# Kernel optimization log

Hardware: AMD Instinct MI355X
Metric: run time of the kernel (lower is better)

Reference implementation:

```python
import jax, jax.numpy as jnp
import numpy as np

N_NODES = 50000
N_EDGES = 1600000
LORA_R = 8


def gcn_conv(h, W, b, src, dst, n):
    # PyG GCNConv: linear transform, add self-loops, symmetric normalization,
    # scatter-add aggregation at target nodes, then bias.
    h = h @ W  # [N, out]
    ones = jnp.ones(src.shape[0], dtype=h.dtype)
    deg = jax.ops.segment_sum(ones, dst, num_segments=n) + 1.0  # +1 for self-loop
    dis = jax.lax.rsqrt(deg)  # deg >= 1 always
    norm = dis[src] * dis[dst]  # [E]
    agg = jax.ops.segment_sum(norm[:, None] * h[src], dst, num_segments=n)
    agg = agg + (dis * dis)[:, None] * h  # self-loop contribution
    return agg + b


def lora(h, A, B):
    # LoRALinear: b(a(x)) * (1/r); replaces input (not additive)
    return (h @ A) @ B * (1.0 / LORA_R)


def setup_inputs() -> dict:
    key = jax.random.key(0)
    ks = jax.random.split(key, 12)
    inp = {}
    inp['x'] = jax.random.normal(ks[0], (N_NODES, 128), dtype=jnp.float32)
    inp['edge_index'] = jax.random.randint(ks[1], (2, N_EDGES), 0, N_NODES, dtype=jnp.int64 if jax.config.jax_enable_x64 else jnp.int32)
    inp['domain_idx'] = jax.random.randint(ks[2], (N_NODES,), 0, 3, dtype=jnp.int32)
    inp['emb_table'] = jax.random.normal(ks[3], (3, 4096), dtype=jnp.float32)
    s1 = 1.0 / np.sqrt(4224.0)
    inp['W1'] = jax.random.normal(ks[4], (4224, 32), dtype=jnp.float32) * s1
    inp['b1'] = jnp.zeros((32,), dtype=jnp.float32)
    inp['A1'] = jax.random.normal(ks[5], (32, LORA_R), dtype=jnp.float32) * (1.0 / np.sqrt(32.0))
    inp['B1'] = jax.random.normal(ks[6], (LORA_R, 32), dtype=jnp.float32) * (1.0 / np.sqrt(LORA_R))
    inp['W2'] = jax.random.normal(ks[7], (32, 5), dtype=jnp.float32) * (1.0 / np.sqrt(32.0))
    inp['b2'] = jnp.zeros((5,), dtype=jnp.float32)
    inp['A2'] = jax.random.normal(ks[8], (5, LORA_R), dtype=jnp.float32) * (1.0 / np.sqrt(5.0))
    inp['B2'] = jax.random.normal(ks[9], (LORA_R, 5), dtype=jnp.float32) * (1.0 / np.sqrt(LORA_R))
    return inp


def reference(x, edge_index, domain_idx, emb_table, W1, b1, A1, B1, W2, b2, A2, B2):
    n = x.shape[0]
    src, dst = edge_index[0], edge_index[1]
    embedded = emb_table[domain_idx]  # [N, 4096]
    h = jnp.concatenate([embedded, x], axis=1)  # [N, 4224]
    h = gcn_conv(h, W1, b1, src, dst, n)
    h = lora(h, A1, B1)
    h = jax.nn.relu(h)
    h = gcn_conv(h, W2, b2, src, dst, n)
    h = lora(h, A2, B2)
    return jax.nn.log_softmax(h, axis=1)
```

## Files before the change

kernel.cpp:

```cpp
#include <hip/hip_runtime.h>
#include <hip/hip_bf16.h>
#include <hip/hip_fp16.h>


#define XDIM 128
#define ODIM 5
#define EMBDIM 4096
#define TB 8192
#define BSH 6
#define BN 64
#define ECAP2 2560

__global__ void __launch_bounds__(256) k_bin(
    const int* __restrict__ src, const int* __restrict__ dst,
    unsigned int* __restrict__ sorted, int* __restrict__ bcur, int e, int ntiles,
    const float* __restrict__ emb, const float* __restrict__ W1,
    float* __restrict__ emb_part) {
    __shared__ unsigned int staged[TB];
    __shared__ int loff[1024], rctr[1024], sbase[1024];
    int t = threadIdx.x;
    if (blockIdx.x >= ntiles) {
        int bx2 = blockIdx.x - ntiles;
        int dm = bx2 >> 5, seg = bx2 & 31;
        const float* er = emb + dm * EMBDIM + seg * 128;
        const float* wr = W1 + (size_t)seg * 128 * 32;
        int j = t & 31, kk = t >> 5;
        float acc = 0.f;
        for (int k2 = kk; k2 < 128; k2 += 8) acc += er[k2] * wr[k2 * 32 + j];
        float* p = (float*)staged;
        p[kk * 32 + j] = acc;
        __syncthreads();
        if (t < 32) {
            float s = 0.f;
            #pragma unroll
            for (int r = 0; r < 8; ++r) s += p[r * 32 + t];
            emb_part[bx2 * 32 + t] = s;
        }
        return;
    }
    int base = blockIdx.x * TB;
    int len = min(TB, e - base);
    for (int i = t; i < 1024; i += 256) { loff[i] = 0; rctr[i] = 0; }
    __syncthreads();
    for (int i = t; i < len; i += 256) atomicAdd(&loff[dst[base + i] >> BSH], 1);
    __syncthreads();
    if (t < 64) {
        int ch = t * 16;
        int v[16]; int s0 = 0;
        #pragma unroll
        for (int k = 0; k < 16; ++k) { v[k] = loff[ch + k]; s0 += v[k]; }
        int pre = s0;
        #pragma unroll
        for (int d2 = 1; d2 < 64; d2 <<= 1) {
            int up = __shfl_up(pre, d2);
            if (t >= d2) pre += up;
        }
        int excl = pre - s0;
        #pragma unroll
        for (int k = 0; k < 16; ++k) { loff[ch + k] = excl; excl += v[k]; }
    }
    __syncthreads();
    for (int i = t; i < len; i += 256) {
        int s = src[base + i], d = dst[base + i];
        int b = d >> BSH;
        int r = atomicAdd(&rctr[b], 1);
        staged[loff[b] + r] = ((unsigned int)d << 16) | (unsigned int)s;
    }
    __syncthreads();
    for (int b = t; b < 1024; b += 256) {
        int l = ((b < 1023) ? loff[b + 1] : len) - loff[b];
        if (l > 0) sbase[b] = atomicAdd(&bcur[b], l);
    }
    __syncthreads();
    for (int i = t; i < len; i += 256) {
        unsigned int u = staged[i];
        int b = (int)(u >> 22);
        int pos = sbase[b] + (i - loff[b]);
        if (pos < ECAP2) sorted[(size_t)b * ECAP2 + pos] = u;
    }
}

__global__ void __launch_bounds__(256) k_disS(
    const unsigned int* __restrict__ sorted, const int* __restrict__ bcur,
    float* __restrict__ dis, int* __restrict__ deg, int n,
    const float* __restrict__ A1, const float* __restrict__ A2,
    const float* __restrict__ B2, const float* __restrict__ b1,
    const float* __restrict__ emb_part, float* __restrict__ M2,
    float* __restrict__ b1A1, float* __restrict__ emb_proj) {
    __shared__ int h[BN];
    int t = threadIdx.x, b = blockIdx.x;
    if (t < BN) h[t] = 0;
    __syncthreads();
    int m = min(bcur[b], ECAP2);
    const unsigned int* sp = sorted + (size_t)b * ECAP2;
    for (int i = t; i < m; i += 256) {
        int d = (int)(sp[i] >> 16);
        atomicAdd(&h[d & (BN - 1)], 1);
    }
    __syncthreads();
    if (t < BN) {
        int node = (b << BSH) + t;
        if (node < n) {
            deg[node] = h[t];
            dis[node] = rsqrtf((float)(h[t] + 1));
        }
    }
    if (b == 0) {
        if (t < 25) {
            int c = t / 5, cp = t % 5;
            float s = 0.f;
            #pragma unroll
            for (int r = 0; r < 8; ++r) s += A2[c * 8 + r] * B2[r * 5 + cp];
            M2[c * 5 + cp] = s * 0.125f;
        }
        if (t >= 32 && t < 40) {
            int j = t - 32;
            float s = 0.f;
            #pragma unroll
            for (int k = 0; k < 32; ++k) s += b1[k] * A1[k * 8 + j];
            b1A1[j] = s;
        }
        if (t >= 64 && t < 160) {
            int d = (t - 64) >> 5, j = (t - 64) & 31;
            float s = 0.f;
            #pragma unroll
            for (int seg = 0; seg < 32; ++seg) s += emb_part[(d * 32 + seg) * 32 + j];
            emb_proj[d * 32 + j] = s;
        }
    }
}

__global__ void __launch_bounds__(256) k_h1(const float* __restrict__ x,
                                            const int* __restrict__ dom,
                                            const float* __restrict__ emb_proj,
                                            const float* __restrict__ W1,
                                            const float* __restrict__ A1,
                                            const float* __restrict__ dis,
                                            float* __restrict__ p1s, int n) {
    __shared__ float wb[XDIM * 32];
    __shared__ float xsT[XDIM * 68];
    __shared__ float sh1[64 * 33];
    __shared__ float sA1[256];
    __shared__ int sdom[64];
    int t = threadIdx.x;
    int row0 = blockIdx.x * 64;
    {
        const float4* w4 = (const float4*)(W1 + (size_t)EMBDIM * 32);
        float4* wb4 = (float4*)wb;
        for (int i = t; i < 1024; i += 256) wb4[i] = w4[i];
    }
    sA1[t] = A1[t];
    if (t < 64) {
        int g = row0 + t;
        sdom[t] = (g < n) ? dom[g] * 32 : 0;
    }
    for (int i = t; i < 2048; i += 256) {
        int c4 = i & 31, row = i >> 5;
        int g = row0 + row;
        float4 v = (g < n) ? ((const float4*)x)[(size_t)g * 32 + c4]
                           : make_float4(0.f, 0.f, 0.f, 0.f);
        int k0 = c4 * 4;
        xsT[(k0 + 0) * 68 + row] = v.x;
        xsT[(k0 + 1) * 68 + row] = v.y;
        xsT[(k0 + 2) * 68 + row] = v.z;
        xsT[(k0 + 3) * 68 + row] = v.w;
    }
    __syncthreads();
    int rq = t >> 4, jp = t & 15;
    float a00 = 0.f, a01 = 0.f, a10 = 0.f, a11 = 0.f;
    float a20 = 0.f, a21 = 0.f, a30 = 0.f, a31 = 0.f;
    #pragma unroll 4
    for (int k = 0; k < XDIM; ++k) {
        float4 xv = *(const float4*)(xsT + k * 68 + rq * 4);
        float2 wv = *(const float2*)(wb + k * 32 + jp * 2);
        a00 += xv.x * wv.x; a01 += xv.x * wv.y;
        a10 += xv.y * wv.x; a11 += xv.y * wv.y;
        a20 += xv.z * wv.x; a21 += xv.z * wv.y;
        a30 += xv.w * wv.x; a31 += xv.w * wv.y;
    }
    int j0 = jp * 2;
    sh1[(rq * 4 + 0) * 33 + j0]     = a00 + emb_proj[sdom[rq * 4 + 0] + j0];
    sh1[(rq * 4 + 0) * 33 + j0 + 1] = a01 + emb_proj[sdom[rq * 4 + 0] + j0 + 1];
    sh1[(rq * 4 + 1) * 33 + j0]     = a10 + emb_proj[sdom[rq * 4 + 1] + j0];
    sh1[(rq * 4 + 1) * 33 + j0 + 1] = a11 + emb_proj[sdom[rq * 4 + 1] + j0 + 1];
    sh1[(rq * 4 + 2) * 33 + j0]     = a20 + emb_proj[sdom[rq * 4 + 2] + j0];
    sh1[(rq * 4 + 2) * 33 + j0 + 1] = a21 + emb_proj[sdom[rq * 4 + 2] + j0 + 1];
    sh1[(rq * 4 + 3) * 33 + j0]     = a30 + emb_proj[sdom[rq * 4 + 3] + j0];
    sh1[(rq * 4 + 3) * 33 + j0 + 1] = a31 + emb_proj[sdom[rq * 4 + 3] + j0 + 1];
    __syncthreads();
    for (int i = t; i < 512; i += 256) {
        int row = i >> 3, jp8 = i & 7;
        int g = row0 + row;
        if (g < n) {
            float s = 0.f;
            #pragma unroll
            for (int kk = 0; kk < 32; ++kk) s += sh1[row * 33 + kk] * sA1[kk * 8 + jp8];
            p1s[(size_t)g * 8 + jp8] = dis[g] * s;
        }
    }
}

__global__ void __launch_bounds__(256) k_bagg1(
    const float* __restrict__ p1s, const unsigned int* __restrict__ sorted,
    const int* __restrict__ bcur, const int* __restrict__ deg,
    const float* __restrict__ dis, const float* __restrict__ b1A1,
    const float* __restrict__ B1, const float* __restrict__ W2,
    float* __restrict__ qs, unsigned short* __restrict__ nsrc, int n) {
    __shared__ unsigned short esrc[ECAP2];
    __shared__ int eoff[BN], sdeg[BN], rctr[BN];
    __shared__ float pacc[3][BN][8];
    __shared__ float sB1[256], sW2[160], sb[8];
    int t = threadIdx.x, b = blockIdx.x;
    int node0 = b << BSH;
    if (t < BN) rctr[t] = 0;
    sB1[t] = B1[t];
    if (t < 160) sW2[t] = W2[t];
    if (t < 8) sb[t] = b1A1[t];
    if (t < 64) {
        int node = node0 + t;
        int v = (node < n) ? deg[node] : 0;
        sdeg[t] = v;
        int pre = v;
        #pragma unroll
        for (int d2 = 1; d2 < 64; d2 <<= 1) {
            int up = __shfl_up(pre, d2);
            if (t >= d2) pre += up;
        }
        eoff[t] = pre - v;
    }
    __syncthreads();
    int m = min(bcur[b], ECAP2);
    const unsigned int* sp = sorted + (size_t)b * ECAP2;
    for (int i = t; i < m; i += 256) {
        unsigned int u = sp[i];
        int dl = (int)(u >> 16) & (BN - 1);
        int r = atomicAdd(&rctr[dl], 1);
        esrc[eoff[dl] + r] = (unsigned short)(u & 0xffffu);
    }
    __syncthreads();
    unsigned short* np = nsrc + (size_t)b * ECAP2;
    for (int i = t; i < m; i += 256) np[i] = esrc[i];
    int nodeL = t & (BN - 1), tsub = t >> BSH;
    int base0 = eoff[nodeL], c = sdeg[nodeL];
    float a[8] = {0.f, 0.f, 0.f, 0.f, 0.f, 0.f, 0.f, 0.f};
    float a2[8] = {0.f, 0.f, 0.f, 0.f, 0.f, 0.f, 0.f, 0.f};
    int k = tsub;
    for (; k + 4 < c; k += 8) {
        int s1 = esrc[base0 + k], s2 = esrc[base0 + k + 4];
        const float4* pr1 = (const float4*)(p1s + s1 * 8);
        const float4* pr2 = (const float4*)(p1s + s2 * 8);
        float4 u0 = pr1[0], u4 = pr1[1], v0 = pr2[0], v4 = pr2[1];
        a[0] += u0.x; a[1] += u0.y; a[2] += u0.z; a[3] += u0.w;
        a[4] += u4.x; a[5] += u4.y; a[6] += u4.z; a[7] += u4.w;
        a2[0] += v0.x; a2[1] += v0.y; a2[2] += v0.z; a2[3] += v0.w;
        a2[4] += v4.x; a2[5] += v4.y; a2[6] += v4.z; a2[7] += v4.w;
    }
    for (; k < c; k += 4) {
        int s1 = esrc[base0 + k];
        const float4* pr1 = (const float4*)(p1s + s1 * 8);
        float4 u0 = pr1[0], u4 = pr1[1];
        a[0] += u0.x; a[1] += u0.y; a[2] += u0.z; a[3] += u0.w;
        a[4] += u4.x; a[5] += u4.y; a[6] += u4.z; a[7] += u4.w;
    }
    #pragma unroll
    for (int j = 0; j < 8; ++j) a[j] += a2[j];
    if (tsub > 0) {
        #pragma unroll
        for (int j = 0; j < 8; ++j) pacc[tsub - 1][nodeL][j] = a[j];
    }
    __syncthreads();
    if (t < BN) {
        int node = node0 + t;
        if (node < n) {
            float dd = dis[node];
            const float4* prn = (const float4*)(p1s + node * 8);
            float4 n0 = prn[0], n4 = prn[1];
            float af[8];
            af[0] = a[0] + n0.x; af[1] = a[1] + n0.y;
            af[2] = a[2] + n0.z; af[3] = a[3] + n0.w;
            af[4] = a[4] + n4.x; af[5] = a[5] + n4.y;
            af[6] = a[6] + n4.z; af[7] = a[7] + n4.w;
            #pragma unroll
            for (int ps = 0; ps < 3; ++ps) {
                #pragma unroll
                for (int j = 0; j < 8; ++j) af[j] += pacc[ps][t][j];
            }
            #pragma unroll
            for (int j = 0; j < 8; ++j) af[j] = dd * af[j] + sb[j];
            float qv[5] = {0.f, 0.f, 0.f, 0.f, 0.f};
            #pragma unroll
            for (int c2 = 0; c2 < 32; ++c2) {
                float tv = 0.f;
                #pragma unroll
                for (int j = 0; j < 8; ++j) tv += af[j] * sB1[j * 32 + c2];
                float st = fmaxf(tv * 0.125f, 0.f);
                #pragma unroll
                for (int o = 0; o < 5; ++o) qv[o] += st * sW2[c2 * 5 + o];
            }
            #pragma unroll
            for (int o = 0; o < 5; ++o) qs[node * 8 + o] = dd * qv[o];
        }
    }
}

__global__ void __launch_bounds__(256) k_bagg2(
    const float* __restrict__ qs, const unsigned short* __restrict__ nsrc,
    const int* __restrict__ bcur, const int* __restrict__ deg,
    const float* __restrict__ dis, const float* __restrict__ b2,
    const float* __restrict__ M2, float* __restrict__ out, int n) {
    __shared__ unsigned short esrc[ECAP2];
    __shared__ int eoff[BN], sdeg[BN];
    __shared__ float pacc[3][BN][5];
    __shared__ float sM2[25], sb2[5];
    int t = threadIdx.x, b = blockIdx.x;
    int node0 = b << BSH;
    if (t < 25) sM2[t] = M2[t];
    if (t < 5) sb2[t] = b2[t];
    if (t < 64) {
        int node = node0 + t;
        int v = (node < n) ? deg[node] : 0;
        sdeg[t] = v;
        int pre = v;
        #pragma unroll
        for (int d2 = 1; d2 < 64; d2 <<= 1) {
            int up = __shfl_up(pre, d2);
            if (t >= d2) pre += up;
        }
        eoff[t] = pre - v;
    }
    __syncthreads();
    int m = min(bcur[b], ECAP2);
    const unsigned short* np = nsrc + (size_t)b * ECAP2;
    for (int i = t; i < m; i += 256) esrc[i] = np[i];
    __syncthreads();
    int nodeL = t & (BN - 1), tsub = t >> BSH;
    int base0 = eoff[nodeL], c = sdeg[nodeL];
    float a[5] = {0.f, 0.f, 0.f, 0.f, 0.f};
    float a2[5] = {0.f, 0.f, 0.f, 0.f, 0.f};
    int k = tsub;
    for (; k + 4 < c; k += 8) {
        int s1 = esrc[base0 + k], s2 = esrc[base0 + k + 4];
        const float4* q1 = (const float4*)(qs + s1 * 8);
        const float4* q2 = (const float4*)(qs + s2 * 8);
        float4 u0 = q1[0]; float u4 = qs[s1 * 8 + 4];
        float4 v0 = q2[0]; float v4 = qs[s2 * 8 + 4];
        a[0] += u0.x; a[1] += u0.y; a[2] += u0.z; a[3] += u0.w; a[4] += u4;
        a2[0] += v0.x; a2[1] += v0.y; a2[2] += v0.z; a2[3] += v0.w; a2[4] += v4;
    }
    for (; k < c; k += 4) {
        int s1 = esrc[base0 + k];
        const float4* q1 = (const float4*)(qs + s1 * 8);
        float4 u0 = q1[0]; float u4 = qs[s1 * 8 + 4];
        a[0] += u0.x; a[1] += u0.y; a[2] += u0.z; a[3] += u0.w; a[4] += u4;
    }
    #pragma unroll
    for (int j = 0; j < 5; ++j) a[j] += a2[j];
    if (tsub > 0) {
        #pragma unroll
        for (int j = 0; j < 5; ++j) pacc[tsub - 1][nodeL][j] = a[j];
    }
    __syncthreads();
    if (t < BN) {
        int node = node0 + t;
        if (node < n) {
            float dd = dis[node];
            const float4* qrn = (const float4*)(qs + node * 8);
            float4 n0 = qrn[0];
            float n4 = qs[node * 8 + 4];
            float av[5];
            av[0] = a[0] + n0.x; av[1] = a[1] + n0.y; av[2] = a[2] + n0.z;
            av[3] = a[3] + n0.w; av[4] = a[4] + n4;
            #pragma unroll
            for (int ps = 0; ps < 3; ++ps) {
                #pragma unroll
                for (int j = 0; j < 5; ++j) av[j] += pacc[ps][t][j];
            }
            #pragma unroll
            for (int j = 0; j < 5; ++j) av[j] = dd * av[j] + sb2[j];
            float z[5];
            #pragma unroll
            for (int cp = 0; cp < 5; ++cp) {
                float s = 0.f;
                #pragma unroll
                for (int c2 = 0; c2 < 5; ++c2) s += av[c2] * sM2[c2 * 5 + cp];
                z[cp] = s;
            }
            float mx = z[0];
            #pragma unroll
            for (int c2 = 1; c2 < 5; ++c2) mx = fmaxf(mx, z[c2]);
            float ssum = 0.f;
            #pragma unroll
            for (int c2 = 0; c2 < 5; ++c2) ssum += __expf(z[c2] - mx);
            float ls = __logf(ssum);
            #pragma unroll
            for (int c2 = 0; c2 < 5; ++c2) out[node * 5 + c2] = z[c2] - mx - ls;
        }
    }
}

extern "C" void kernel_launch(void* const* d_in, const int* in_sizes, int n_in,
                              void* d_out, int out_size, void* d_ws, size_t ws_size,
                              hipStream_t stream) {
    const float* x   = (const float*)d_in[0];
    const int*   ei  = (const int*)d_in[1];
    const int*   dom = (const int*)d_in[2];
    const float* emb = (const float*)d_in[3];
    const float* W1  = (const float*)d_in[4];
    const float* b1  = (const float*)d_in[5];
    const float* A1  = (const float*)d_in[6];
    const float* B1  = (const float*)d_in[7];
    const float* W2  = (const float*)d_in[8];
    const float* b2  = (const float*)d_in[9];
    const float* A2  = (const float*)d_in[10];
    const float* B2  = (const float*)d_in[11];
    float* out = (float*)d_out;

    int n = in_sizes[2];
    int e = in_sizes[1] / 2;
    const int* src = ei;
    const int* dst = ei + e;

    int ntiles = (e + TB - 1) / TB;
    int nbuck  = (n + BN - 1) >> BSH;

    char* base = (char*)d_ws;
    size_t o = 0;
    auto carve = [&](size_t bytes) {
        void* p = base + o;
        o = (o + bytes + 15) & ~(size_t)15;
        return p;
    };
    float* emb_part = (float*)carve(96 * 32 * sizeof(float));
    float* emb_proj = (float*)carve(3 * 32 * sizeof(float));
    float* M2       = (float*)carve(32 * sizeof(float));
    float* b1A1     = (float*)carve(8 * sizeof(float));
    float* dis      = (float*)carve((size_t)n * sizeof(float));
    int*   deg      = (int*)carve((size_t)n * sizeof(int));
    float* p1s      = (float*)carve((size_t)n * 8 * sizeof(float));
    float* qs       = (float*)carve((size_t)n * 8 * sizeof(float));
    int*   bcur     = (int*)carve(1024 * sizeof(int));
    unsigned int* sorted = (unsigned int*)carve((size_t)nbuck * ECAP2 * sizeof(unsigned int));
    unsigned short* nsrc = (unsigned short*)carve((size_t)nbuck * ECAP2 * sizeof(unsigned short));
    (void)ws_size; (void)n_in; (void)out_size;

    hipMemsetAsync(bcur, 0, 1024 * sizeof(int), stream);

    k_bin<<<ntiles + 96, 256, 0, stream>>>(src, dst, sorted, bcur, e, ntiles,
                                           emb, W1, emb_part);
    k_disS<<<nbuck, 256, 0, stream>>>(sorted, bcur, dis, deg, n,
                                      A1, A2, B2, b1, emb_part, M2, b1A1, emb_proj);
    k_h1<<<nbuck, 256, 0, stream>>>(x, dom, emb_proj, W1, A1, dis, p1s, n);
    k_bagg1<<<nbuck, 256, 0, stream>>>(p1s, sorted, bcur, deg, dis, b1A1, B1, W2, qs, nsrc, n);
    k_bagg2<<<nbuck, 256, 0, stream>>>(qs, nsrc, bcur, deg, dis, b2, M2, out, n);
}
```

Before: 177.7 us.

## Fuse all five GCN stages into one persistent cooperative kernel with grid syncs

```diff
diff --git a/kernel.cpp b/kernel.cpp
--- a/kernel.cpp
+++ b/kernel.cpp
@@ -1,399 +1,412 @@
 #include <hip/hip_runtime.h>
 #include <hip/hip_bf16.h>
 #include <hip/hip_fp16.h>
+#include <hip/hip_cooperative_groups.h>
+
+namespace cg = cooperative_groups;
 
 
 #define XDIM 128
-#define ODIM 5
 #define EMBDIM 4096
 #define TB 8192
 #define BSH 6
 #define BN 64
 #define ECAP2 2560
 
-__global__ void __launch_bounds__(256) k_bin(
-    const int* __restrict__ src, const int* __restrict__ dst,
-    unsigned int* __restrict__ sorted, int* __restrict__ bcur, int e, int ntiles,
-    const float* __restrict__ emb, const float* __restrict__ W1,
-    float* __restrict__ emb_part) {
-    __shared__ unsigned int staged[TB];
-    __shared__ int loff[1024], rctr[1024], sbase[1024];
-    int t = threadIdx.x;
-    if (blockIdx.x >= ntiles) {
-        int bx2 = blockIdx.x - ntiles;
-        int dm = bx2 >> 5, seg = bx2 & 31;
-        const float* er = emb + dm * EMBDIM + seg * 128;
-        const float* wr = W1 + (size_t)seg * 128 * 32;
-        int j = t & 31, kk = t >> 5;
-        float acc = 0.f;
-        for (int k2 = kk; k2 < 128; k2 += 8) acc += er[k2] * wr[k2 * 32 + j];
-        float* p = (float*)staged;
-        p[kk * 32 + j] = acc;
-        __syncthreads();
-        if (t < 32) {
-            float s = 0.f;
+#define SMEM_A 16384
+#define SMEM_B 36096
+
+struct Prm {
+    const float* x; const int* src; const int* dst; const int* dom;
+    const float* emb; const float* W1; const float* b1; const float* A1;
+    const float* B1; const float* W2; const float* b2; const float* A2; const float* B2;
+    float* out;
+    float* emb_part; float* emb_proj; float* M2; float* b1A1;
+    int* deg; float* p1s; float* qs; int* bcur;
+    unsigned int* sorted; unsigned short* nsrc;
+    int n, e, ntiles, nbuck;
+};
+
+__global__ void __launch_bounds__(256, 3) k_fused(Prm p) {
+    __shared__ __align__(16) char smem[SMEM_A + SMEM_B];
+    cg::grid_group gg = cg::this_grid();
+    const int t = threadIdx.x;
+    const int bx = blockIdx.x;
+    const int G = gridDim.x;
+    const int gtid = bx * 256 + t;
+    const int gsz = G * 256;
+
+    for (int i = gtid; i < 1024; i += gsz) p.bcur[i] = 0;
+    for (int i = gtid; i < p.n; i += gsz) p.deg[i] = 0;
+    {
+        float* red = (float*)smem;
+        for (int c = bx; c < 97; c += G) {
+            if (c < 96) {
+                int dm = c >> 5, seg = c & 31;
+                const float* er = p.emb + dm * EMBDIM + seg * 128;
+                const float* wr = p.W1 + (size_t)(seg * 128) * 32;
+                int j = t & 31, kk = t >> 5;
+                float acc = 0.f;
+                for (int k2 = kk; k2 < 128; k2 += 8) acc += er[k2] * wr[k2 * 32 + j];
+                __syncthreads();
+                red[kk * 32 + j] = acc;
+                __syncthreads();
+                if (t < 32) {
+                    float s = 0.f;
+                    #pragma unroll
+                    for (int r = 0; r < 8; ++r) s += red[r * 32 + t];
+                    p.emb_part[c * 32 + t] = s;
+                }
+            } else {
+                if (t < 25) {
+                    int c5 = t / 5, cp = t % 5;
+                    float s = 0.f;
+                    #pragma unroll
+                    for (int r = 0; r < 8; ++r) s += p.A2[c5 * 8 + r] * p.B2[r * 5 + cp];
+                    p.M2[c5 * 5 + cp] = s * 0.125f;
+                }
+                if (t >= 32 && t < 40) {
+                    int j = t - 32;
+                    float s = 0.f;
+                    #pragma unroll
+                    for (int k = 0; k < 32; ++k) s += p.b1[k] * p.A1[k * 8 + j];
+                    p.b1A1[j] = s;
+                }
+            }
+        }
+    }
+    gg.sync();
+
+    {
+        unsigned int* staged = (unsigned int*)(smem + SMEM_A);
+        int* loff  = (int*)smem;
+        int* rctr  = (int*)(smem + 4096);
+        int* sbase = (int*)(smem + 8192);
+        for (int tile = bx; tile < p.ntiles + 1; tile += G) {
+            if (tile < p.ntiles) {
+                int base = tile * TB;
+                int len = min(TB, p.e - base);
+                __syncthreads();
+                for (int i = t; i < 1024; i += 256) { loff[i] = 0; rctr[i] = 0; }
+                __syncthreads();
+                for (int i = t; i < len; i += 256) {
+                    int d = p.dst[base + i];
+                    atomicAdd(&loff[d >> BSH], 1);
+                    atomicAdd(&p.deg[d], 1);
+                }
+                __syncthreads();
+                if (t < 64) {
+                    int ch = t * 16;
+                    int v[16]; int s0 = 0;
+                    #pragma unroll
+                    for (int k = 0; k < 16; ++k) { v[k] = loff[ch + k]; s0 += v[k]; }
+                    int pre = s0;
+                    #pragma unroll
+                    for (int d2 = 1; d2 < 64; d2 <<= 1) {
+                        int up = __shfl_up(pre, d2);
+                        if (t >= d2) pre += up;
+                    }
+                    int excl = pre - s0;
+                    #pragma unroll
+                    for (int k = 0; k < 16; ++k) { loff[ch + k] = excl; excl += v[k]; }
+                }
+                __syncthreads();
+                for (int i = t; i < len; i += 256) {
+                    int s = p.src[base + i], d = p.dst[base + i];
+                    int b = d >> BSH;
+                    int r = atomicAdd(&rctr[b], 1);
+                    staged[loff[b] + r] = ((unsigned int)d << 16) | (unsigned int)s;
+                }
+                __syncthreads();
+                for (int b2 = t; b2 < 1024; b2 += 256) {
+                    int l = ((b2 < 1023) ? loff[b2 + 1] : len) - loff[b2];
+                    if (l > 0) sbase[b2] = atomicAdd(&p.bcur[b2], l);
+                }
+                __syncthreads();
+                for (int i = t; i < len; i += 256) {
+                    unsigned int u = staged[i];
+                    int b2 = (int)(u >> 22);
+                    int pos = sbase[b2] + (i - loff[b2]);
+                    if (pos < ECAP2) p.sorted[(size_t)b2 * ECAP2 + pos] = u;
+                }
+            } else {
+                if (t < 96) {
+                    int d = t >> 5, j = t & 31;
+                    float s = 0.f;
+                    #pragma unroll
+                    for (int seg = 0; seg < 32; ++seg) s += p.emb_part[(d * 32 + seg) * 32 + j];
+                    p.emb_proj[d * 32 + j] = s;
+                }
+            }
+        }
+    }
+    gg.sync();
+
+    {
+        float* wb   = (float*)smem;
+        float* xsT  = (float*)(smem + SMEM_A);
+        float* sh1  = xsT;
+        float* sA1  = (float*)(smem + SMEM_A + 34816);
+        int*   sdom = (int*)(smem + SMEM_A + 34816 + 1024);
+        {
+            const float4* w4 = (const float4*)(p.W1 + (size_t)EMBDIM * 32);
+            float4* wb4 = (float4*)wb;
+            for (int i = t; i < 1024; i += 256) wb4[i] = w4[i];
+            sA1[t] = p.A1[t];
+        }
+        for (int c = bx; c < p.nbuck; c += G) {
+            int row0 = c * 64;
+            __syncthreads();
+            if (t < 64) {
+                int g = row0 + t;
+                sdom[t] = (g < p.n) ? p.dom[g] * 32 : 0;
+            }
+            for (int i = t; i < 2048; i += 256) {
+                int c4 = i & 31, row = i >> 5;
+                int g = row0 + row;
+                float4 v = (g < p.n) ? ((const float4*)p.x)[(size_t)g * 32 + c4]
+                                     : make_float4(0.f, 0.f, 0.f, 0.f);
+                int k0 = c4 * 4;
+                xsT[(k0 + 0) * 68 + row] = v.x;
+                xsT[(k0 + 1) * 68 + row] = v.y;
+                xsT[(k0 + 2) * 68 + row] = v.z;
+                xsT[(k0 + 3) * 68 + row] = v.w;
+            }
+            __syncthreads();
+            int rq = t >> 4, jp = t & 15;
+            float a00 = 0.f, a01 = 0.f, a10 = 0.f, a11 = 0.f;
+            float a20 = 0.f, a21 = 0.f, a30 = 0.f, a31 = 0.f;
+            #pragma unroll 4
+            for (int k = 0; k < XDIM; ++k) {
+                float4 xv = *(const float4*)(xsT + k * 68 + rq * 4);
+                float2 wv = *(const float2*)(wb + k * 32 + jp * 2);
+                a00 += xv.x * wv.x; a01 += xv.x * wv.y;
+                a10 += xv.y * wv.x; a11 += xv.y * wv.y;
+                a20 += xv.z * wv.x; a21 += xv.z * wv.y;
+                a30 += xv.w * wv.x; a31 += xv.w * wv.y;
+            }
+            __syncthreads();
+            int j0 = jp * 2;
+            sh1[(rq * 4 + 0) * 33 + j0]     = a00 + p.emb_proj[sdom[rq * 4 + 0] + j0];
+            sh1[(rq * 4 + 0) * 33 + j0 + 1] = a01 + p.emb_proj[sdom[rq * 4 + 0] + j0 + 1];
+            sh1[(rq * 4 + 1) * 33 + j0]     = a10 + p.emb_proj[sdom[rq * 4 + 1] + j0];
+            sh1[(rq * 4 + 1) * 33 + j0 + 1] = a11 + p.emb_proj[sdom[rq * 4 + 1] + j0 + 1];
+            sh1[(rq * 4 + 2) * 33 + j0]     = a20 + p.emb_proj[sdom[rq * 4 + 2] + j0];
+            sh1[(rq * 4 + 2) * 33 + j0 + 1] = a21 + p.emb_proj[sdom[rq * 4 + 2] + j0 + 1];
+            sh1[(rq * 4 + 3) * 33 + j0]     = a30 + p.emb_proj[sdom[rq * 4 + 3] + j0];
+            sh1[(rq * 4 + 3) * 33 + j0 + 1] = a31 + p.emb_proj[sdom[rq * 4 + 3] + j0 + 1];
+            __syncthreads();
+            for (int i = t; i < 512; i += 256) {
+                int row = i >> 3, jp8 = i & 7;
+                int g = row0 + row;
+                if (g < p.n) {
+                    float s = 0.f;
+                    #pragma unroll
+                    for (int kk = 0; kk < 32; ++kk) s += sh1[row * 33 + kk] * sA1[kk * 8 + jp8];
+                    float dd = rsqrtf((float)(p.deg[g] + 1));
+                    p.p1s[(size_t)g * 8 + jp8] = dd * s;
+                }
+            }
+        }
+    }
+    gg.sync();
+
+    {
+        float* sB1 = (float*)smem;
+        float* sW2 = (float*)(smem + 1024);
+        float* sb  = (float*)(smem + 1664);
+        unsigned short* esrc = (unsigned short*)(smem + SMEM_A);
+        float* pacc = (float*)(smem + SMEM_A + 5120);
+        int* eoff = (int*)(smem + SMEM_A + 5120 + 6144);
+        int* sdeg = eoff + 64;
+        int* rctr = sdeg + 64;
+        sB1[t] = p.B1[t];
+        if (t < 160) sW2[t] = p.W2[t];
+        if (t < 8) sb[t] = p.b1A1[t];
+        for (int b = bx; b < p.nbuck; b += G) {
+            int node0 = b << BSH;
+            __syncthreads();
+            if (t < 64) {
+                int node = node0 + t;
+                int v = (node < p.n) ? p.deg[node] : 0;
+                sdeg[t] = v; rctr[t] = 0;
+                int pre = v;
+                #pragma unroll
+                for (int d2 = 1; d2 < 64; d2 <<= 1) {
+                    int up = __shfl_up(pre, d2);
+                    if (t >= d2) pre += up;
+                }
+                eoff[t] = pre - v;
+            }
+            __syncthreads();
+            int m = min(p.bcur[b], ECAP2);
+            const unsigned int* sp = p.sorted + (size_t)b * ECAP2;
+            for (int i = t; i < m; i += 256) {
+                unsigned int u = sp[i];
+                int dl = (int)(u >> 16) & (BN - 1);
+                int r = atomicAdd(&rctr[dl], 1);
+                esrc[eoff[dl] + r] = (unsigned short)(u & 0xffffu);
+            }
+            __syncthreads();
+            unsigned short* np = p.nsrc + (size_t)b * ECAP2;
+            for (int i = t; i < m; i += 256) np[i] = esrc[i];
+            int nodeL = t & (BN - 1), tsub = t >> BSH;
+            int base0 = eoff[nodeL], c = sdeg[nodeL];
+            float a[8] = {0.f, 0.f, 0.f, 0.f, 0.f, 0.f, 0.f, 0.f};
+            float a2[8] = {0.f, 0.f, 0.f, 0.f, 0.f, 0.f, 0.f, 0.f};
+            int k = tsub;
+            for (; k + 4 < c; k += 8) {
+                int s1 = esrc[base0 + k], s2 = esrc[base0 + k + 4];
+                const float4* pr1 = (const float4*)(p.p1s + s1 * 8);
+                const float4* pr2 = (const float4*)(p.p1s + s2 * 8);
+                float4 u0 = pr1[0], u4 = pr1[1], v0 = pr2[0], v4 = pr2[1];
+                a[0] += u0.x; a[1] += u0.y; a[2] += u0.z; a[3] += u0.w;
+                a[4] += u4.x; a[5] += u4.y; a[6] += u4.z; a[7] += u4.w;
+                a2[0] += v0.x; a2[1] += v0.y; a2[2] += v0.z; a2[3] += v0.w;
+                a2[4] += v4.x; a2[5] += v4.y; a2[6] += v4.z; a2[7] += v4.w;
+            }
+            for (; k < c; k += 4) {
+                int s1 = esrc[base0 + k];
+                const float4* pr1 = (const float4*)(p.p1s + s1 * 8);
+                float4 u0 = pr1[0], u4 = pr1[1];
+                a[0] += u0.x; a[1] += u0.y; a[2] += u0.z; a[3] += u0.w;
+                a[4] += u4.x; a[5] += u4.y; a[6] += u4.z; a[7] += u4.w;
+            }
             #pragma unroll
-            for (int r = 0; r < 8; ++r) s += p[r * 32 + t];
-            emb_part[bx2 * 32 + t] = s;
-        }
-        return;
+            for (int j = 0; j < 8; ++j) a[j] += a2[j];
+            if (tsub > 0) {
+                #pragma unroll
+                for (int j = 0; j < 8; ++j) pacc[((tsub - 1) * BN + nodeL) * 8 + j] = a[j];
+            }
+            __syncthreads();
+            if (t < BN) {
+                int node = node0 + t;
+                if (node < p.n) {
+                    float dd = rsqrtf((float)(sdeg[t] + 1));
+                    const float4* prn = (const float4*)(p.p1s + node * 8);
+                    float4 n0 = prn[0], n4 = prn[1];
+                    float af[8];
+                    af[0] = a[0] + n0.x; af[1] = a[1] + n0.y;
+                    af[2] = a[2] + n0.z; af[3] = a[3] + n0.w;
+                    af[4] = a[4] + n4.x; af[5] = a[5] + n4.y;
+                    af[6] = a[6] + n4.z; af[7] = a[7] + n4.w;
+                    #pragma unroll
+                    for (int ps = 0; ps < 3; ++ps) {
+                        #pragma unroll
+                        for (int j = 0; j < 8; ++j) af[j] += pacc[(ps * BN + t) * 8 + j];
+                    }
+                    #pragma unroll
+                    for (int j = 0; j < 8; ++j) af[j] = dd * af[j] + sb[j];
+                    float qv[5] = {0.f, 0.f, 0.f, 0.f, 0.f};
+                    #pragma unroll
+                    for (int c2 = 0; c2 < 32; ++c2) {
+                        float tv = 0.f;
+                        #pragma unroll
+                        for (int j = 0; j < 8; ++j) tv += af[j] * sB1[j * 32 + c2];
+                        float st = fmaxf(tv * 0.125f, 0.f);
+                        #pragma unroll
+                        for (int o = 0; o < 5; ++o) qv[o] += st * sW2[c2 * 5 + o];
+                    }
+                    #pragma unroll
+                    for (int o = 0; o < 5; ++o) p.qs[node * 8 + o] = dd * qv[o];
+                }
+            }
+        }
     }
-    int base = blockIdx.x * TB;
-    int len = min(TB, e - base);
-    for (int i = t; i < 1024; i += 256) { loff[i] = 0; rctr[i] = 0; }
-    __syncthreads();
-    for (int i = t; i < len; i += 256) atomicAdd(&loff[dst[base + i] >> BSH], 1);
-    __syncthreads();
-    if (t < 64) {
-        int ch = t * 16;
-        int v[16]; int s0 = 0;
-        #pragma unroll
-        for (int k = 0; k < 16; ++k) { v[k] = loff[ch + k]; s0 += v[k]; }
-        int pre = s0;
-        #pragma unroll
-        for (int d2 = 1; d2 < 64; d2 <<= 1) {
-            int up = __shfl_up(pre, d2);
-            if (t >= d2) pre += up;
-        }
-        int excl = pre - s0;
-        #pragma unroll
-        for (int k = 0; k < 16; ++k) { loff[ch + k] = excl; excl += v[k]; }
-    }
-    __syncthreads();
-    for (int i = t; i < len; i += 256) {
-        int s = src[base + i], d = dst[base + i];
-        int b = d >> BSH;
-        int r = atomicAdd(&rctr[b], 1);
-        staged[loff[b] + r] = ((unsigned int)d << 16) | (unsigned int)s;
-    }
-    __syncthreads();
-    for (int b = t; b < 1024; b += 256) {
-        int l = ((b < 1023) ? loff[b + 1] : len) - loff[b];
-        if (l > 0) sbase[b] = atomicAdd(&bcur[b], l);
-    }
-    __syncthreads();
-    for (int i = t; i < len; i += 256) {
-        unsigned int u = staged[i];
-        int b = (int)(u >> 22);
-        int pos = sbase[b] + (i - loff[b]);
-        if (pos < ECAP2) sorted[(size_t)b * ECAP2 + pos] = u;
-    }
-}
-
-__global__ void __launch_bounds__(256) k_disS(
-    const unsigned int* __restrict__ sorted, const int* __restrict__ bcur,
-    float* __restrict__ dis, int* __restrict__ deg, int n,
-    const float* __restrict__ A1, const float* __restrict__ A2,
-    const float* __restrict__ B2, const float* __restrict__ b1,
-    const float* __restrict__ emb_part, float* __restrict__ M2,
-    float* __restrict__ b1A1, float* __restrict__ emb_proj) {
-    __shared__ int h[BN];
-    int t = threadIdx.x, b = blockIdx.x;
-    if (t < BN) h[t] = 0;
-    __syncthreads();
-    int m = min(bcur[b], ECAP2);
-    const unsigned int* sp = sorted + (size_t)b * ECAP2;
-    for (int i = t; i < m; i += 256) {
-        int d = (int)(sp[i] >> 16);
-        atomicAdd(&h[d & (BN - 1)], 1);
-    }
-    __syncthreads();
-    if (t < BN) {
-        int node = (b << BSH) + t;
-        if (node < n) {
-            deg[node] = h[t];
-            dis[node] = rsqrtf((float)(h[t] + 1));
-        }
-    }
-    if (b == 0) {
-        if (t < 25) {
-            int c = t / 5, cp = t % 5;
-            float s = 0.f;
+    gg.sync();
+
+    {
+        float* sM2 = (float*)smem;
+        float* sb2 = (float*)(smem + 128);
+        unsigned short* esrc = (unsigned short*)(smem + SMEM_A);
+        float* pacc = (float*)(smem + SMEM_A + 5120);
+        int* eoff = (int*)(smem + SMEM_A + 5120 + 3840);
+        int* sdeg = eoff + 64;
+        if (t < 25) sM2[t] = p.M2[t];
+        if (t < 5) sb2[t] = p.b2[t];
+        for (int b = bx; b < p.nbuck; b += G) {
+            int node0 = b << BSH;
+            __syncthreads();
+            if (t < 64) {
+                int node = node0 + t;
+                int v = (node < p.n) ? p.deg[node] : 0;
+                sdeg[t] = v;
+                int pre = v;
+                #pragma unroll
+                for (int d2 = 1; d2 < 64; d2 <<= 1) {
+                    int up = __shfl_up(pre, d2);
+                    if (t >= d2) pre += up;
+                }
+                eoff[t] = pre - v;
+            }
+            __syncthreads();
+            int m = min(p.bcur[b], ECAP2);
+            const unsigned short* np = p.nsrc + (size_t)b * ECAP2;
+            for (int i = t; i < m; i += 256) esrc[i] = np[i];
+            __syncthreads();
+            int nodeL = t & (BN - 1), tsub = t >> BSH;
+            int base0 = eoff[nodeL], c = sdeg[nodeL];
+            float a[5] = {0.f, 0.f, 0.f, 0.f, 0.f};
+            float a2[5] = {0.f, 0.f, 0.f, 0.f, 0.f};
+            int k = tsub;
+            for (; k + 4 < c; k += 8) {
+                int s1 = esrc[base0 + k], s2 = esrc[base0 + k + 4];
+                const float4* q1 = (const float4*)(p.qs + s1 * 8);
+                const float4* q2 = (const float4*)(p.qs + s2 * 8);
+                float4 u0 = q1[0]; float u4 = p.qs[s1 * 8 + 4];
+                float4 v0 = q2[0]; float v4 = p.qs[s2 * 8 + 4];
+                a[0] += u0.x; a[1] += u0.y; a[2] += u0.z; a[3] += u0.w; a[4] += u4;
+                a2[0] += v0.x; a2[1] += v0.y; a2[2] += v0.z; a2[3] += v0.w; a2[4] += v4;
+            }
+            for (; k < c; k += 4) {
+                int s1 = esrc[base0 + k];
+                const float4* q1 = (const float4*)(p.qs + s1 * 8);
+                float4 u0 = q1[0]; float u4 = p.qs[s1 * 8 + 4];
+                a[0] += u0.x; a[1] += u0.y; a[2] += u0.z; a[3] += u0.w; a[4] += u4;
+            }
             #pragma unroll
-            for (int r = 0; r < 8; ++r) s += A2[c * 8 + r] * B2[r * 5 + cp];
-            M2[c * 5 + cp] = s * 0.125f;
-        }
-        if (t >= 32 && t < 40) {
-            int j = t - 32;
-            float s = 0.f;
-            #pragma unroll
-            for (int k = 0; k < 32; ++k) s += b1[k] * A1[k * 8 + j];
-            b1A1[j] = s;
-        }
-        if (t >= 64 && t < 160) {
-            int d = (t - 64) >> 5, j = (t - 64) & 31;
-            float s = 0.f;
-            #pragma unroll
-            for (int seg = 0; seg < 32; ++seg) s += emb_part[(d * 32 + seg) * 32 + j];
-            emb_proj[d * 32 + j] = s;
-        }
-    }
-}
-
-__global__ void __launch_bounds__(256) k_h1(const float* __restrict__ x,
-                                            const int* __restrict__ dom,
-                                            const float* __restrict__ emb_proj,
-                                            const float* __restrict__ W1,
-                                            const float* __restrict__ A1,
-                                            const float* __restrict__ dis,
-                                            float* __restrict__ p1s, int n) {
-    __shared__ float wb[XDIM * 32];
-    __shared__ float xsT[XDIM * 68];
-    __shared__ float sh1[64 * 33];
-    __shared__ float sA1[256];
-    __shared__ int sdom[64];
-    int t = threadIdx.x;
-    int row0 = blockIdx.x * 64;
-    {
-        const float4* w4 = (const float4*)(W1 + (size_t)EMBDIM * 32);
-        float4* wb4 = (float4*)wb;
-        for (int i = t; i < 1024; i += 256) wb4[i] = w4[i];
-    }
-    sA1[t] = A1[t];
-    if (t < 64) {
-        int g = row0 + t;
-        sdom[t] = (g < n) ? dom[g] * 32 : 0;
-    }
-    for (int i = t; i < 2048; i += 256) {
-        int c4 = i & 31, row = i >> 5;
-        int g = row0 + row;
-        float4 v = (g < n) ? ((const float4*)x)[(size_t)g * 32 + c4]
-                           : make_float4(0.f, 0.f, 0.f, 0.f);
-        int k0 = c4 * 4;
-        xsT[(k0 + 0) * 68 + row] = v.x;
-        xsT[(k0 + 1) * 68 + row] = v.y;
-        xsT[(k0 + 2) * 68 + row] = v.z;
-        xsT[(k0 + 3) * 68 + row] = v.w;
-    }
-    __syncthreads();
-    int rq = t >> 4, jp = t & 15;
-    float a00 = 0.f, a01 = 0.f, a10 = 0.f, a11 = 0.f;
-    float a20 = 0.f, a21 = 0.f, a30 = 0.f, a31 = 0.f;
-    #pragma unroll 4
-    for (int k = 0; k < XDIM; ++k) {
-        float4 xv = *(const float4*)(xsT + k * 68 + rq * 4);
-        float2 wv = *(const float2*)(wb + k * 32 + jp * 2);
-        a00 += xv.x * wv.x; a01 += xv.x * wv.y;
-        a10 += xv.y * wv.x; a11 += xv.y * wv.y;
-        a20 += xv.z * wv.x; a21 += xv.z * wv.y;
-        a30 += xv.w * wv.x; a31 += xv.w * wv.y;
-    }
-    int j0 = jp * 2;
-    sh1[(rq * 4 + 0) * 33 + j0]     = a00 + emb_proj[sdom[rq * 4 + 0] + j0];
-    sh1[(rq * 4 + 0) * 33 + j0 + 1] = a01 + emb_proj[sdom[rq * 4 + 0] + j0 + 1];
-    sh1[(rq * 4 + 1) * 33 + j0]     = a10 + emb_proj[sdom[rq * 4 + 1] + j0];
-    sh1[(rq * 4 + 1) * 33 + j0 + 1] = a11 + emb_proj[sdom[rq * 4 + 1] + j0 + 1];
-    sh1[(rq * 4 + 2) * 33 + j0]     = a20 + emb_proj[sdom[rq * 4 + 2] + j0];
-    sh1[(rq * 4 + 2) * 33 + j0 + 1] = a21 + emb_proj[sdom[rq * 4 + 2] + j0 + 1];
-    sh1[(rq * 4 + 3) * 33 + j0]     = a30 + emb_proj[sdom[rq * 4 + 3] + j0];
-    sh1[(rq * 4 + 3) * 33 + j0 + 1] = a31 + emb_proj[sdom[rq * 4 + 3] + j0 + 1];
-    __syncthreads();
-    for (int i = t; i < 512; i += 256) {
-        int row = i >> 3, jp8 = i & 7;
-        int g = row0 + row;
-        if (g < n) {
-            float s = 0.f;
-            #pragma unroll
-            for (int kk = 0; kk < 32; ++kk) s += sh1[row * 33 + kk] * sA1[kk * 8 + jp8];
-            p1s[(size_t)g * 8 + jp8] = dis[g] * s;
-        }
-    }
-}
-
-__global__ void __launch_bounds__(256) k_bagg1(
-    const float* __restrict__ p1s, const unsigned int* __restrict__ sorted,
-    const int* __restrict__ bcur, const int* __restrict__ deg,
-    const float* __restrict__ dis, const float* __restrict__ b1A1,
-    const float* __restrict__ B1, const float* __restrict__ W2,
-    float* __restrict__ qs, unsigned short* __restrict__ nsrc, int n) {
-    __shared__ unsigned short esrc[ECAP2];
-    __shared__ int eoff[BN], sdeg[BN], rctr[BN];
-    __shared__ float pacc[3][BN][8];
-    __shared__ float sB1[256], sW2[160], sb[8];
-    int t = threadIdx.x, b = blockIdx.x;
-    int node0 = b << BSH;
-    if (t < BN) rctr[t] = 0;
-    sB1[t] = B1[t];
-    if (t < 160) sW2[t] = W2[t];
-    if (t < 8) sb[t] = b1A1[t];
-    if (t < 64) {
-        int node = node0 + t;
-        int v = (node < n) ? deg[node] : 0;
-        sdeg[t] = v;
-        int pre = v;
-        #pragma unroll
-        for (int d2 = 1; d2 < 64; d2 <<= 1) {
-            int up = __shfl_up(pre, d2);
-            if (t >= d2) pre += up;
-        }
-        eoff[t] = pre - v;
-    }
-    __syncthreads();
-    int m = min(bcur[b], ECAP2);
-    const unsigned int* sp = sorted + (size_t)b * ECAP2;
-    for (int i = t; i < m; i += 256) {
-        unsigned int u = sp[i];
-        int dl = (int)(u >> 16) & (BN - 1);
-        int r = atomicAdd(&rctr[dl], 1);
-        esrc[eoff[dl] + r] = (unsigned short)(u & 0xffffu);
-    }
-    __syncthreads();
-    unsigned short* np = nsrc + (size_t)b * ECAP2;
-    for (int i = t; i < m; i += 256) np[i] = esrc[i];
-    int nodeL = t & (BN - 1), tsub = t >> BSH;
-    int base0 = eoff[nodeL], c = sdeg[nodeL];
-    float a[8] = {0.f, 0.f, 0.f, 0.f, 0.f, 0.f, 0.f, 0.f};
-    float a2[8] = {0.f, 0.f, 0.f, 0.f, 0.f, 0.f, 0.f, 0.f};
-    int k = tsub;
-    for (; k + 4 < c; k += 8) {
-        int s1 = esrc[base0 + k], s2 = esrc[base0 + k + 4];
-        const float4* pr1 = (const float4*)(p1s + s1 * 8);
-        const float4* pr2 = (const float4*)(p1s + s2 * 8);
-        float4 u0 = pr1[0], u4 = pr1[1], v0 = pr2[0], v4 = pr2[1];
-        a[0] += u0.x; a[1] += u0.y; a[2] += u0.z; a[3] += u0.w;
-        a[4] += u4.x; a[5] += u4.y; a[6] += u4.z; a[7] += u4.w;
-        a2[0] += v0.x; a2[1] += v0.y; a2[2] += v0.z; a2[3] += v0.w;
-        a2[4] += v4.x; a2[5] += v4.y; a2[6] += v4.z; a2[7] += v4.w;
-    }
-    for (; k < c; k += 4) {
-        int s1 = esrc[base0 + k];
-        const float4* pr1 = (const float4*)(p1s + s1 * 8);
-        float4 u0 = pr1[0], u4 = pr1[1];
-        a[0] += u0.x; a[1] += u0.y; a[2] += u0.z; a[3] += u0.w;
-        a[4] += u4.x; a[5] += u4.y; a[6] += u4.z; a[7] += u4.w;
-    }
-    #pragma unroll
-    for (int j = 0; j < 8; ++j) a[j] += a2[j];
-    if (tsub > 0) {
-        #pragma unroll
-        for (int j = 0; j < 8; ++j) pacc[tsub - 1][nodeL][j] = a[j];
-    }
-    __syncthreads();
-    if (t < BN) {
-        int node = node0 + t;
-        if (node < n) {
-            float dd = dis[node];
-            const float4* prn = (const float4*)(p1s + node * 8);
-            float4 n0 = prn[0], n4 = prn[1];
-            float af[8];
-            af[0] = a[0] + n0.x; af[1] = a[1] + n0.y;
-            af[2] = a[2] + n0.z; af[3] = a[3] + n0.w;
-            af[4] = a[4] + n4.x; af[5] = a[5] + n4.y;
-            af[6] = a[6] + n4.z; af[7] = a[7] + n4.w;
-            #pragma unroll
-            for (int ps = 0; ps < 3; ++ps) {
+            for (int j = 0; j < 5; ++j) a[j] += a2[j];
+            if (tsub > 0) {
                 #pragma unroll
-                for (int j = 0; j < 8; ++j) af[j] += pacc[ps][t][j];
-            }
-            #pragma unroll
-            for (int j = 0; j < 8; ++j) af[j] = dd * af[j] + sb[j];
-            float qv[5] = {0.f, 0.f, 0.f, 0.f, 0.f};
-            #pragma unroll
-            for (int c2 = 0; c2 < 32; ++c2) {
-                float tv = 0.f;
-                #pragma unroll
-                for (int j = 0; j < 8; ++j) tv += af[j] * sB1[j * 32 + c2];
-                float st = fmaxf(tv * 0.125f, 0.f);
-                #pragma unroll
-                for (int o = 0; o < 5; ++o) qv[o] += st * sW2[c2 * 5 + o];
-            }
-            #pragma unroll
-            for (int o = 0; o < 5; ++o) qs[node * 8 + o] = dd * qv[o];
-        }
-    }
-}
-
-__global__ void __launch_bounds__(256) k_bagg2(
-    const float* __restrict__ qs, const unsigned short* __restrict__ nsrc,
-    const int* __restrict__ bcur, const int* __restrict__ deg,
-    const float* __restrict__ dis, const float* __restrict__ b2,
-    const float* __restrict__ M2, float* __restrict__ out, int n) {
-    __shared__ unsigned short esrc[ECAP2];
-    __shared__ int eoff[BN], sdeg[BN];
-    __shared__ float pacc[3][BN][5];
-    __shared__ float sM2[25], sb2[5];
-    int t = threadIdx.x, b = blockIdx.x;
-    int node0 = b << BSH;
-    if (t < 25) sM2[t] = M2[t];
-    if (t < 5) sb2[t] = b2[t];
-    if (t < 64) {
-        int node = node0 + t;
-        int v = (node < n) ? deg[node] : 0;
-        sdeg[t] = v;
-        int pre = v;
-        #pragma unroll
-        for (int d2 = 1; d2 < 64; d2 <<= 1) {
-            int up = __shfl_up(pre, d2);
-            if (t >= d2) pre += up;
-        }
-        eoff[t] = pre - v;
-    }
-    __syncthreads();
-    int m = min(bcur[b], ECAP2);
-    const unsigned short* np = nsrc + (size_t)b * ECAP2;
-    for (int i = t; i < m; i += 256) esrc[i] = np[i];
-    __syncthreads();
-    int nodeL = t & (BN - 1), tsub = t >> BSH;
-    int base0 = eoff[nodeL], c = sdeg[nodeL];
-    float a[5] = {0.f, 0.f, 0.f, 0.f, 0.f};
-    float a2[5] = {0.f, 0.f, 0.f, 0.f, 0.f};
-    int k = tsub;
-    for (; k + 4 < c; k += 8) {
-        int s1 = esrc[base0 + k], s2 = esrc[base0 + k + 4];
-        const float4* q1 = (const float4*)(qs + s1 * 8);
-        const float4* q2 = (const float4*)(qs + s2 * 8);
-        float4 u0 = q1[0]; float u4 = qs[s1 * 8 + 4];
-        float4 v0 = q2[0]; float v4 = qs[s2 * 8 + 4];
-        a[0] += u0.x; a[1] += u0.y; a[2] += u0.z; a[3] += u0.w; a[4] += u4;
-        a2[0] += v0.x; a2[1] += v0.y; a2[2] += v0.z; a2[3] += v0.w; a2[4] += v4;
-    }
-    for (; k < c; k += 4) {
-        int s1 = esrc[base0 + k];
-        const float4* q1 = (const float4*)(qs + s1 * 8);
-        float4 u0 = q1[0]; float u4 = qs[s1 * 8 + 4];
-        a[0] += u0.x; a[1] += u0.y; a[2] += u0.z; a[3] += u0.w; a[4] += u4;
-    }
-    #pragma unroll
-    for (int j = 0; j < 5; ++j) a[j] += a2[j];
-    if (tsub > 0) {
-        #pragma unroll
-        for (int j = 0; j < 5; ++j) pacc[tsub - 1][nodeL][j] = a[j];
-    }
-    __syncthreads();
-    if (t < BN) {
-        int node = node0 + t;
-        if (node < n) {
-            float dd = dis[node];
-            const float4* qrn = (const float4*)(qs + node * 8);
-            float4 n0 = qrn[0];
-            float n4 = qs[node * 8 + 4];
-            float av[5];
-            av[0] = a[0] + n0.x; av[1] = a[1] + n0.y; av[2] = a[2] + n0.z;
-            av[3] = a[3] + n0.w; av[4] = a[4] + n4;
-            #pragma unroll
-            for (int ps = 0; ps < 3; ++ps) {
-                #pragma unroll
-                for (int j = 0; j < 5; ++j) av[j] += pacc[ps][t][j];
-            }
-            #pragma unroll
-            for (int j = 0; j < 5; ++j) av[j] = dd * av[j] + sb2[j];
-            float z[5];
-            #pragma unroll
-            for (int cp = 0; cp < 5; ++cp) {
-                float s = 0.f;
-                #pragma unroll
-                for (int c2 = 0; c2 < 5; ++c2) s += av[c2] * sM2[c2 * 5 + cp];
-                z[cp] = s;
-            }
-            float mx = z[0];
-            #pragma unroll
-            for (int c2 = 1; c2 < 5; ++c2) mx = fmaxf(mx, z[c2]);
-            float ssum = 0.f;
-            #pragma unroll
-            for (int c2 = 0; c2 < 5; ++c2) ssum += __expf(z[c2] - mx);
-            float ls = __logf(ssum);
-            #pragma unroll
-            for (int c2 = 0; c2 < 5; ++c2) out[node * 5 + c2] = z[c2] - mx - ls;
+                for (int j = 0; j < 5; ++j) pacc[((tsub - 1) * BN + nodeL) * 5 + j] = a[j];
+            }
+            __syncthreads();
+            if (t < BN) {
+                int node = node0 + t;
+                if (node < p.n) {
+                    float dd = rsqrtf((float)(sdeg[t] + 1));
+                    const float4* qrn = (const float4*)(p.qs + node * 8);
+                    float4 n0 = qrn[0];
+                    float n4 = p.qs[node * 8 + 4];
+                    float av[5];
+                    av[0] = a[0] + n0.x; av[1] = a[1] + n0.y; av[2] = a[2] + n0.z;
+                    av[3] = a[3] + n0.w; av[4] = a[4] + n4;
+                    #pragma unroll
+                    for (int ps = 0; ps < 3; ++ps) {
+                        #pragma unroll
+                        for (int j = 0; j < 5; ++j) av[j] += pacc[(ps * BN + t) * 5 + j];
+                    }
+                    #pragma unroll
+                    for (int j = 0; j < 5; ++j) av[j] = dd * av[j] + sb2[j];
+                    float z[5];
+                    #pragma unroll
+                    for (int cp = 0; cp < 5; ++cp) {
+                        float s = 0.f;
+                        #pragma unroll
+                        for (int c2 = 0; c2 < 5; ++c2) s += av[c2] * sM2[c2 * 5 + cp];
+                        z[cp] = s;
+                    }
+                    float mx = z[0];
+                    #pragma unroll
+                    for (int c2 = 1; c2 < 5; ++c2) mx = fmaxf(mx, z[c2]);
+                    float ssum = 0.f;
+                    #pragma unroll
+                    for (int c2 = 0; c2 < 5; ++c2) ssum += __expf(z[c2] - mx);
+                    float ls = __logf(ssum);
+                    #pragma unroll
+                    for (int c2 = 0; c2 < 5; ++c2) p.out[node * 5 + c2] = z[c2] - mx - ls;
+                }
+            }
         }
     }
 }
@@ -401,55 +414,53 @@
 extern "C" void kernel_launch(void* const* d_in, const int* in_sizes, int n_in,
                               void* d_out, int out_size, void* d_ws, size_t ws_size,
                               hipStream_t stream) {
-    const float* x   = (const float*)d_in[0];
-    const int*   ei  = (const int*)d_in[1];
-    const int*   dom = (const int*)d_in[2];
-    const float* emb = (const float*)d_in[3];
-    const float* W1  = (const float*)d_in[4];
-    const float* b1  = (const float*)d_in[5];
-    const float* A1  = (const float*)d_in[6];
-    const float* B1  = (const float*)d_in[7];
-    const float* W2  = (const float*)d_in[8];
-    const float* b2  = (const float*)d_in[9];
-    const float* A2  = (const float*)d_in[10];
-    const float* B2  = (const float*)d_in[11];
-    float* out = (float*)d_out;
-
-    int n = in_sizes[2];
-    int e = in_sizes[1] / 2;
-    const int* src = ei;
-    const int* dst = ei + e;
-
-    int ntiles = (e + TB - 1) / TB;
-    int nbuck  = (n + BN - 1) >> BSH;
+    Prm p;
+    p.x   = (const float*)d_in[0];
+    const int* ei = (const int*)d_in[1];
+    p.dom = (const int*)d_in[2];
+    p.emb = (const float*)d_in[3];
+    p.W1  = (const float*)d_in[4];
+    p.b1  = (const float*)d_in[5];
+    p.A1  = (const float*)d_in[6];
+    p.B1  = (const float*)d_in[7];
+    p.W2  = (const float*)d_in[8];
+    p.b2  = (const float*)d_in[9];
+    p.A2  = (const float*)d_in[10];
+    p.B2  = (const float*)d_in[11];
+    p.out = (float*)d_out;
+
+    p.n = in_sizes[2];
+    p.e = in_sizes[1] / 2;
+    p.src = ei;
+    p.dst = ei + p.e;
+    p.ntiles = (p.e + TB - 1) / TB;
+    p.nbuck  = (p.n + BN - 1) >> BSH;
 
     char* base = (char*)d_ws;
     size_t o = 0;
     auto carve = [&](size_t bytes) {
-        void* p = base + o;
+        void* ptr = base + o;
         o = (o + bytes + 15) & ~(size_t)15;
-        return p;
+        return ptr;
     };
-    float* emb_part = (float*)carve(96 * 32 * sizeof(float));
-    float* emb_proj = (float*)carve(3 * 32 * sizeof(float));
-    float* M2       = (float*)carve(32 * sizeof(float));
-    float* b1A1     = (float*)carve(8 * sizeof(float));
-    float* dis      = (float*)carve((size_t)n * sizeof(float));
-    int*   deg      = (int*)carve((size_t)n * sizeof(int));
-    float* p1s      = (float*)carve((size_t)n * 8 * sizeof(float));
-    float* qs       = (float*)carve((size_t)n * 8 * sizeof(float));
-    int*   bcur     = (int*)carve(1024 * sizeof(int));
-    unsigned int* sorted = (unsigned int*)carve((size_t)nbuck * ECAP2 * sizeof(unsigned int));
-    unsigned short* nsrc = (unsigned short*)carve((size_t)nbuck * ECAP2 * sizeof(unsigned short));
+    p.emb_part = (float*)carve(96 * 32 * sizeof(float));
+    p.emb_proj = (float*)carve(3 * 32 * sizeof(float));
+    p.M2       = (float*)carve(32 * sizeof(float));
+    p.b1A1     = (float*)carve(8 * sizeof(float));
+    p.deg      = (int*)carve((size_t)p.n * sizeof(int));
+    p.p1s      = (float*)carve((size_t)p.n * 8 * sizeof(float));
+    p.qs       = (float*)carve((size_t)p.n * 8 * sizeof(float));
+    p.bcur     = (int*)carve(1024 * sizeof(int));
+    p.sorted   = (unsigned int*)carve((size_t)p.nbuck * ECAP2 * sizeof(unsigned int));
+    p.nsrc     = (unsigned short*)carve((size_t)p.nbuck * ECAP2 * sizeof(unsigned short));
     (void)ws_size; (void)n_in; (void)out_size;
 
-    hipMemsetAsync(bcur, 0, 1024 * sizeof(int), stream);
-
-    k_bin<<<ntiles + 96, 256, 0, stream>>>(src, dst, sorted, bcur, e, ntiles,
-                                           emb, W1, emb_part);
-    k_disS<<<nbuck, 256, 0, stream>>>(sorted, bcur, dis, deg, n,
-                                      A1, A2, B2, b1, emb_part, M2, b1A1, emb_proj);
-    k_h1<<<nbuck, 256, 0, stream>>>(x, dom, emb_proj, W1, A1, dis, p1s, n);
-    k_bagg1<<<nbuck, 256, 0, stream>>>(p1s, sorted, bcur, deg, dis, b1A1, B1, W2, qs, nsrc, n);
-    k_bagg2<<<nbuck, 256, 0, stream>>>(qs, nsrc, bcur, deg, dis, b2, M2, out, n);
+    int maxB = 0;
+    hipError_t err = hipOccupancyMaxActiveBlocksPerMultiprocessor(&maxB, k_fused, 256, 0);
+    if (err != hipSuccess || maxB < 1) maxB = 2;
+    int G = maxB * 256;
+    if (G > p.nbuck) G = p.nbuck;
+
+    void* args[] = {&p};
+    hipLaunchCooperativeKernel((void*)k_fused, dim3(G), dim3(256), args, 0, stream);
 }
```

Result: slower. 385.7 us (+117.1%).
